# Optimization experiments

Measured on AMD Instinct MI355X. Metric: run time of the kernel, lower is better.

The kernel has to match this reference:

```python
import jax, jax.numpy as jnp
import numpy as np

N_NODES = 50000
N_EDGES = 800000
VOCAB = 500
IN_DIM = 128
HID = 128
OUT_DIM = 64
N_GRAPHS = 512


def setup_inputs() -> dict:
    key = jax.random.key(0)
    ks = jax.random.split(key, 12)
    s = 0.05
    return {
        "emb": jax.random.normal(ks[0], (VOCAB, IN_DIM), jnp.float32) * s,
        "w1a": jax.random.normal(ks[1], (HID, IN_DIM), jnp.float32) * s,
        "b1a": jnp.zeros((HID,), jnp.float32),
        "w1b": jax.random.normal(ks[2], (HID, HID), jnp.float32) * s,
        "b1b": jnp.zeros((HID,), jnp.float32),
        "w2a": jax.random.normal(ks[3], (HID, HID), jnp.float32) * s,
        "b2a": jnp.zeros((HID,), jnp.float32),
        "w2b": jax.random.normal(ks[4], (HID, HID), jnp.float32) * s,
        "b2b": jnp.zeros((HID,), jnp.float32),
        "fc_w": jax.random.normal(ks[5], (OUT_DIM, HID), jnp.float32) * s,
        "fc_b": jnp.zeros((OUT_DIM,), jnp.float32),
        "x_idx": jax.random.randint(ks[6], (N_NODES,), 0, VOCAB, jnp.int32),
        "edge_index": jax.random.randint(ks[7], (2, N_EDGES), 0, N_NODES, jnp.int32),
        "batch": jnp.sort(jax.random.randint(ks[8], (N_NODES,), 0, N_GRAPHS, jnp.int32)),
    }


def gin_conv(x, wa, ba, wb, bb, src, dst):
    # GINConv with eps=0: MLP(x + sum_{j->i} x_j)
    agg = jax.ops.segment_sum(x[src], dst, num_segments=N_NODES)  # [N, d]
    h = x + agg
    h = jax.nn.relu(h @ wa.T + ba)
    return h @ wb.T + bb


def reference(emb, w1a, b1a, w1b, b1b, w2a, b2a, w2b, b2b, fc_w, fc_b,
              x_idx, edge_index, batch):
    src, dst = edge_index[0], edge_index[1]
    x = emb[x_idx]  # [N, IN_DIM] embedding lookup
    x = jax.nn.relu(gin_conv(x, w1a, b1a, w1b, b1b, src, dst))
    x = jax.nn.relu(gin_conv(x, w2a, b2a, w2b, b2b, src, dst))
    # global mean pool over graphs
    sums = jax.ops.segment_sum(x, batch, num_segments=N_GRAPHS)  # [G, HID]
    cnt = jax.ops.segment_sum(jnp.ones((N_NODES,), x.dtype), batch, num_segments=N_GRAPHS)
    pooled = sums / jnp.maximum(cnt, 1.0)[:, None]
    return pooled @ fc_w.T + fc_b  # [G, OUT_DIM]
```

## Files before the change

### kernel.cpp

```cpp
#include <hip/hip_runtime.h>

#define N_NODES 50000
#define N_EDGES 800000
#define DIM 128
#define NGRAPH 512
#define ODIM 64
#define VOCAB 500
#define NBKT 391
#define NB2 128
#define EPB2 (N_EDGES / NB2)
#define CAP 4096

typedef __attribute__((ext_vector_type(8))) short bf16x8;
typedef __attribute__((ext_vector_type(4))) short bf16x4;
typedef __attribute__((ext_vector_type(4))) float f32x4;

__device__ inline unsigned short f2bf(float f) {
  unsigned u = __builtin_bit_cast(unsigned, f);
  return (unsigned short)((u + 0x7fffu + ((u >> 16) & 1u)) >> 16);
}
__device__ inline float bf2f(unsigned short h) {
  unsigned u = ((unsigned)h) << 16;
  return __builtin_bit_cast(float, u);
}

__global__ __launch_bounds__(256) void emb2bf_kernel(
    const float* __restrict__ emb, unsigned short* __restrict__ embb) {
  int i = blockIdx.x * 256 + threadIdx.x;
  if (i >= VOCAB * 16) return;
  const f32x4* src = (const f32x4*)(emb + (size_t)i * 8);
  f32x4 a = src[0], b = src[1];
  bf16x8 o;
  #pragma unroll
  for (int e = 0; e < 4; ++e) {
    o[e] = (short)f2bf(a[e]);
    o[4 + e] = (short)f2bf(b[e]);
  }
  *(bf16x8*)(embb + (size_t)i * 8) = o;
}

__global__ __launch_bounds__(256) void w2bf_kernel(
    const float* __restrict__ w1a, const float* __restrict__ w1b,
    const float* __restrict__ w2a, const float* __restrict__ w2b,
    unsigned short* __restrict__ wbf) {
  int u = blockIdx.x * 256 + threadIdx.x;
  if (u >= 4 * 2048) return;
  int m = u >> 11, loc = u & 2047;
  const float* src = (m == 0) ? w1a : (m == 1) ? w1b : (m == 2) ? w2a : w2b;
  const f32x4* sp = (const f32x4*)(src + (size_t)loc * 8);
  f32x4 a = sp[0], b = sp[1];
  bf16x8 o;
  #pragma unroll
  for (int e = 0; e < 4; ++e) {
    o[e] = (short)f2bf(a[e]);
    o[4 + e] = (short)f2bf(b[e]);
  }
  *(bf16x8*)(wbf + (size_t)u * 8) = o;
}

__global__ __launch_bounds__(512) void bkt_hist_kernel(
    const int* __restrict__ ei, unsigned* __restrict__ HB) {
  __shared__ unsigned cnt[NBKT];
  int t = threadIdx.x, b = blockIdx.x;
  for (int i = t; i < NBKT; i += 512) cnt[i] = 0;
  __syncthreads();
  int base = b * EPB2;
  for (int i = t; i < EPB2; i += 512)
    atomicAdd(&cnt[(unsigned)ei[N_EDGES + base + i] >> 7], 1u);
  __syncthreads();
  for (int i = t; i < NBKT; i += 512) HB[(size_t)b * NBKT + i] = cnt[i];
}

__global__ __launch_bounds__(128) void col_scan_kernel(
    const unsigned* __restrict__ HB, unsigned* __restrict__ OFF,
    unsigned* __restrict__ tot) {
  __shared__ unsigned w0s;
  int k = blockIdx.x, t = threadIdx.x;
  int lane = t & 63, wid = t >> 6;
  unsigned v = HB[(size_t)t * NBKT + k];
  unsigned s = v;
  #pragma unroll
  for (int d = 1; d < 64; d <<= 1) {
    unsigned u = __shfl_up(s, d, 64);
    if (lane >= d) s += u;
  }
  if (wid == 0 && lane == 63) w0s = s;
  __syncthreads();
  unsigned excl = s - v + (wid ? w0s : 0u);
  OFF[(size_t)t * NBKT + k] = excl;
  if (t == 127) tot[k] = excl + v;
}

__global__ __launch_bounds__(512) void base_scan_kernel(
    const unsigned* __restrict__ tot, int* __restrict__ bktbase,
    int* __restrict__ row) {
  __shared__ unsigned wsum[8];
  int t = threadIdx.x;
  int lane = t & 63, wid = t >> 6;
  unsigned v = (t < NBKT) ? tot[t] : 0u;
  unsigned s = v;
  #pragma unroll
  for (int d = 1; d < 64; d <<= 1) {
    unsigned u = __shfl_up(s, d, 64);
    if (lane >= d) s += u;
  }
  if (lane == 63) wsum[wid] = s;
  __syncthreads();
  if (wid == 0) {
    unsigned ws = (lane < 8) ? wsum[lane] : 0u;
    #pragma unroll
    for (int d = 1; d < 8; d <<= 1) {
      unsigned u = __shfl_up(ws, d, 64);
      if (lane >= d) ws += u;
    }
    if (lane < 8) wsum[lane] = ws;
  }
  __syncthreads();
  unsigned excl = s - v + (wid ? wsum[wid - 1] : 0u);
  if (t < NBKT) bktbase[t] = (int)excl;
  if (t == NBKT - 1) {
    bktbase[NBKT] = (int)(excl + v);
    row[N_NODES] = N_EDGES;
  }
}

__global__ __launch_bounds__(512) void bkt_scatter_kernel(
    const int* __restrict__ ei, const unsigned* __restrict__ OFF,
    const int* __restrict__ bktbase, unsigned* __restrict__ eb) {
  __shared__ unsigned cur[NBKT];
  int t = threadIdx.x, b = blockIdx.x;
  for (int i = t; i < NBKT; i += 512)
    cur[i] = OFF[(size_t)b * NBKT + i] + (unsigned)bktbase[i];
  __syncthreads();
  int base = b * EPB2;
  for (int i = t; i < EPB2; i += 512) {
    int s = ei[base + i];
    unsigned d = (unsigned)ei[N_EDGES + base + i];
    unsigned pos = atomicAdd(&cur[d >> 7], 1u);
    eb[pos] = ((d & 127u) << 16) | (unsigned)s;
  }
}

__global__ __launch_bounds__(256) void sort_bucket_kernel(
    const unsigned* __restrict__ eb, const int* __restrict__ bktbase,
    int* __restrict__ srt, int* __restrict__ row) {
  __shared__ unsigned stage[CAP];
  __shared__ unsigned short sorted[CAP];
  __shared__ unsigned hist[128], excl[128], cur[128];
  __shared__ unsigned wtot;
  int t = threadIdx.x, bkt = blockIdx.x;
  int base = bktbase[bkt], end = bktbase[bkt + 1];
  int cnt = end - base;
  if (cnt > CAP) cnt = CAP;
  if (t < 128) hist[t] = 0;
  __syncthreads();
  for (int i = t; i < cnt; i += 256) {
    unsigned e = eb[base + i];
    stage[i] = e;
    atomicAdd(&hist[e >> 16], 1u);
  }
  __syncthreads();
  if (t < 128) {
    int lane = t & 63;
    unsigned v = hist[t], s = v;
    #pragma unroll
    for (int d = 1; d < 64; d <<= 1) {
      unsigned u = __shfl_up(s, d, 64);
      if (lane >= d) s += u;
    }
    if (t == 63) wtot = s;
    excl[t] = s - v;
  }
  __syncthreads();
  if (t < 128) {
    unsigned e0 = excl[t] + (t >= 64 ? wtot : 0u);
    cur[t] = e0;
    int n = bkt * 128 + t;
    if (n < N_NODES) row[n] = base + (int)e0;
  }
  __syncthreads();
  for (int i = t; i < cnt; i += 256) {
    unsigned e = stage[i];
    unsigned r = atomicAdd(&cur[e >> 16], 1u);
    sorted[r] = (unsigned short)(e & 0xFFFFu);
  }
  __syncthreads();
  for (int i = t; i < cnt; i += 256) srt[base + i] = (int)sorted[i];
}

__global__ __launch_bounds__(256) void agg_emb_kernel(
    const unsigned short* __restrict__ embb, const int* __restrict__ xidx,
    const int* __restrict__ row, const int* __restrict__ srt,
    unsigned short* __restrict__ xa) {
  int n = blockIdx.x * 16 + (threadIdx.x >> 4);
  int c = threadIdx.x & 15;
  int lo = row[n], hi = row[n + 1];
  bf16x8 sv = *(const bf16x8*)(embb + (size_t)xidx[n] * DIM + c * 8);
  float a[8];
  #pragma unroll
  for (int e = 0; e < 8; ++e) a[e] = bf2f((unsigned short)sv[e]);
  int k = lo;
  for (; k + 8 <= hi; k += 8) {
    bf16x8 w[8];
    #pragma unroll
    for (int q = 0; q < 8; ++q)
      w[q] = *(const bf16x8*)(embb + (size_t)xidx[srt[k + q]] * DIM + c * 8);
    #pragma unroll
    for (int q = 0; q < 8; ++q)
      #pragma unroll
      for (int e = 0; e < 8; ++e) a[e] += bf2f((unsigned short)w[q][e]);
  }
  for (; k + 2 <= hi; k += 2) {
    bf16x8 w0 = *(const bf16x8*)(embb + (size_t)xidx[srt[k]] * DIM + c * 8);
    bf16x8 w1 = *(const bf16x8*)(embb + (size_t)xidx[srt[k + 1]] * DIM + c * 8);
    #pragma unroll
    for (int e = 0; e < 8; ++e)
      a[e] += bf2f((unsigned short)w0[e]) + bf2f((unsigned short)w1[e]);
  }
  if (k < hi) {
    bf16x8 w = *(const bf16x8*)(embb + (size_t)xidx[srt[k]] * DIM + c * 8);
    #pragma unroll
    for (int e = 0; e < 8; ++e) a[e] += bf2f((unsigned short)w[e]);
  }
  bf16x8 o;
  #pragma unroll
  for (int e = 0; e < 8; ++e) o[e] = (short)f2bf(a[e]);
  *(bf16x8*)(xa + (size_t)n * DIM + c * 8) = o;
}

__global__ __launch_bounds__(256) void agg_x_kernel(
    const unsigned short* __restrict__ x, const int* __restrict__ row,
    const int* __restrict__ srt, unsigned short* __restrict__ xa) {
  int n = blockIdx.x * 16 + (threadIdx.x >> 4);
  int c = threadIdx.x & 15;
  int lo = row[n], hi = row[n + 1];
  bf16x8 sv = *(const bf16x8*)(x + (size_t)n * DIM + c * 8);
  float a[8];
  #pragma unroll
  for (int e = 0; e < 8; ++e) a[e] = bf2f((unsigned short)sv[e]);
  int k = lo;
  for (; k + 8 <= hi; k += 8) {
    bf16x8 w[8];
    #pragma unroll
    for (int q = 0; q < 8; ++q)
      w[q] = *(const bf16x8*)(x + (size_t)srt[k + q] * DIM + c * 8);
    #pragma unroll
    for (int q = 0; q < 8; ++q)
      #pragma unroll
      for (int e = 0; e < 8; ++e) a[e] += bf2f((unsigned short)w[q][e]);
  }
  for (; k + 2 <= hi; k += 2) {
    bf16x8 w0 = *(const bf16x8*)(x + (size_t)srt[k] * DIM + c * 8);
    bf16x8 w1 = *(const bf16x8*)(x + (size_t)srt[k + 1] * DIM + c * 8);
    #pragma unroll
    for (int e = 0; e < 8; ++e)
      a[e] += bf2f((unsigned short)w0[e]) + bf2f((unsigned short)w1[e]);
  }
  if (k < hi) {
    bf16x8 w = *(const bf16x8*)(x + (size_t)srt[k] * DIM + c * 8);
    #pragma unroll
    for (int e = 0; e < 8; ++e) a[e] += bf2f((unsigned short)w[e]);
  }
  bf16x8 o;
  #pragma unroll
  for (int e = 0; e < 8; ++e) o[e] = (short)f2bf(a[e]);
  *(bf16x8*)(xa + (size_t)n * DIM + c * 8) = o;
}

__global__ __launch_bounds__(256) void mlp_mfma_kernel(
    const unsigned short* __restrict__ xa,
    const unsigned short* __restrict__ wabf, const float* __restrict__ ba,
    const unsigned short* __restrict__ wbbf, const float* __restrict__ bb,
    unsigned short* __restrict__ xout) {
  __shared__ short Xs[64 * 128];
  __shared__ short Hs[64 * 128];
  int t = threadIdx.x;
  int lane = t & 63;
  int w = t >> 6;
  int jq = w * 32;
  int l15 = lane & 15;
  int lg = lane >> 4;
  int nbase = blockIdx.x * 64;

  bf16x8 waf[2][4], wbf[2][4];
  #pragma unroll
  for (int jm = 0; jm < 2; ++jm) {
    int jrow = jq + jm * 16 + l15;
    #pragma unroll
    for (int ks = 0; ks < 4; ++ks) {
      int k0 = ks * 32 + lg * 8;
      waf[jm][ks] = *(const bf16x8*)(wabf + (size_t)jrow * DIM + k0);
      wbf[jm][ks] = *(const bf16x8*)(wbbf + (size_t)jrow * DIM + k0);
    }
  }
  f32x4 ba_r[2], bb_r[2];
  #pragma unroll
  for (int jm = 0; jm < 2; ++jm) {
    ba_r[jm] = *(const f32x4*)(ba + jq + jm * 16 + lg * 4);
    bb_r[jm] = *(const f32x4*)(bb + jq + jm * 16 + lg * 4);
  }

  {
    int r = t >> 2;
    int cb = (t & 3) * 4;
    int node = nbase + r;
    #pragma unroll
    for (int i = 0; i < 4; ++i) {
      int chunk = cb + i;
      bf16x8 v = {0, 0, 0, 0, 0, 0, 0, 0};
      if (node < N_NODES)
        v = *(const bf16x8*)(xa + (size_t)node * DIM + chunk * 8);
      *(bf16x8*)&Xs[r * 128 + ((chunk ^ (r & 7)) << 3)] = v;
    }
  }
  __syncthreads();

  #pragma unroll
  for (int nt = 0; nt < 4; ++nt) {
    int rrow = nt * 16 + l15;
    bf16x8 xf[4];
    #pragma unroll
    for (int ks = 0; ks < 4; ++ks) {
      int chunk = ks * 4 + lg;
      xf[ks] = *(const bf16x8*)&Xs[rrow * 128 + ((chunk ^ (rrow & 7)) << 3)];
    }
    #pragma unroll
    for (int jm = 0; jm < 2; ++jm) {
      f32x4 acc = ba_r[jm];
      #pragma unroll
      for (int ks = 0; ks < 4; ++ks)
        acc = __builtin_amdgcn_mfma_f32_16x16x32_bf16(waf[jm][ks], xf[ks], acc, 0, 0, 0);
      int hnode = nt * 16 + l15;
      int cbase = jq + jm * 16 + lg * 4;
      unsigned p0 = (unsigned)f2bf(fmaxf(acc[0], 0.f)) |
                    ((unsigned)f2bf(fmaxf(acc[1], 0.f)) << 16);
      unsigned p1 = (unsigned)f2bf(fmaxf(acc[2], 0.f)) |
                    ((unsigned)f2bf(fmaxf(acc[3], 0.f)) << 16);
      unsigned idx = hnode * 128 + (((cbase >> 3) ^ (hnode & 7)) << 3) + (cbase & 7);
      *(uint2*)&Hs[idx] = make_uint2(p0, p1);
    }
  }
  __syncthreads();

  #pragma unroll
  for (int nt = 0; nt < 4; ++nt) {
    int rrow = nt * 16 + l15;
    bf16x8 hf[4];
    #pragma unroll
    for (int ks = 0; ks < 4; ++ks) {
      int chunk = ks * 4 + lg;
      hf[ks] = *(const bf16x8*)&Hs[rrow * 128 + ((chunk ^ (rrow & 7)) << 3)];
    }
    #pragma unroll
    for (int jm = 0; jm < 2; ++jm) {
      f32x4 acc = bb_r[jm];
      #pragma unroll
      for (int ks = 0; ks < 4; ++ks)
        acc = __builtin_amdgcn_mfma_f32_16x16x32_bf16(wbf[jm][ks], hf[ks], acc, 0, 0, 0);
      int node = nbase + nt * 16 + l15;
      if (node < N_NODES) {
        bf16x4 o;
        #pragma unroll
        for (int e = 0; e < 4; ++e) o[e] = (short)f2bf(fmaxf(acc[e], 0.f));
        *(bf16x4*)(xout + (size_t)node * DIM + jq + jm * 16 + lg * 4) = o;
      }
    }
  }
}

#define PP 132
__global__ __launch_bounds__(256) void pool_fc_kernel(
    const unsigned short* __restrict__ x, const int* __restrict__ batch,
    const float* __restrict__ fcw, const float* __restrict__ fcb,
    float* __restrict__ out) {
  int g = blockIdx.x, t = threadIdx.x;
  __shared__ float part[16 * PP];
  __shared__ float pooled[DIM];
  __shared__ int sbound[2];
  if (t < 2) {
    int target = g + t;
    int lo = 0, hi = N_NODES;
    while (lo < hi) {
      int m = (lo + hi) >> 1;
      if (batch[m] < target) lo = m + 1; else hi = m;
    }
    sbound[t] = lo;
  }
  __syncthreads();
  int lo = sbound[0], hi = sbound[1];
  int r = t >> 4, c = t & 15;
  float acc[8] = {0.f, 0.f, 0.f, 0.f, 0.f, 0.f, 0.f, 0.f};
  for (int nn = lo + r; nn < hi; nn += 16) {
    bf16x8 v = *(const bf16x8*)(x + (size_t)nn * DIM + c * 8);
    #pragma unroll
    for (int e = 0; e < 8; ++e) acc[e] += bf2f((unsigned short)v[e]);
  }
  #pragma unroll
  for (int e = 0; e < 8; ++e) part[r * PP + c * 8 + e] = acc[e];
  __syncthreads();
  if (t < DIM) {
    float s = 0.f;
    #pragma unroll
    for (int rr = 0; rr < 16; ++rr) s += part[rr * PP + t];
    pooled[t] = s / fmaxf((float)(hi - lo), 1.0f);
  }
  __syncthreads();
  if (t < ODIM) {
    float a = fcb[t];
    const float* wr = fcw + (size_t)t * DIM;
    #pragma unroll 8
    for (int h = 0; h < DIM; ++h) a += pooled[h] * wr[h];
    out[(size_t)g * ODIM + t] = a;
  }
}

extern "C" void kernel_launch(void* const* d_in, const int* in_sizes, int n_in,
                              void* d_out, int out_size, void* d_ws, size_t ws_size,
                              hipStream_t stream) {
  const float* emb  = (const float*)d_in[0];
  const float* w1a  = (const float*)d_in[1];
  const float* b1a  = (const float*)d_in[2];
  const float* w1b  = (const float*)d_in[3];
  const float* b1b  = (const float*)d_in[4];
  const float* w2a  = (const float*)d_in[5];
  const float* b2a  = (const float*)d_in[6];
  const float* w2b  = (const float*)d_in[7];
  const float* b2b  = (const float*)d_in[8];
  const float* fcw  = (const float*)d_in[9];
  const float* fcb  = (const float*)d_in[10];
  const int*   xidx = (const int*)d_in[11];
  const int*   ei   = (const int*)d_in[12];
  const int*   batch= (const int*)d_in[13];
  float* out = (float*)d_out;

  size_t featb = (size_t)N_NODES * DIM * sizeof(unsigned short);
  char* ws = (char*)d_ws;
  unsigned short* B1 = (unsigned short*)ws;
  unsigned short* B2 = (unsigned short*)(ws + featb);
  char* p = ws + 2 * featb;
  unsigned short* embb = (unsigned short*)p;  p += (VOCAB * DIM * 2 + 15) / 16 * 16;
  unsigned short* wbf  = (unsigned short*)p;  p += (4 * DIM * DIM * 2 + 15) / 16 * 16;
  int* row  = (int*)p;      p += ((N_NODES + 1) * 4 + 15) / 16 * 16;
  int* bktbase = (int*)p;   p += ((NBKT + 1) * 4 + 15) / 16 * 16;
  unsigned* HB  = (unsigned*)p;  p += (size_t)NB2 * NBKT * 4;
  unsigned* OFF = (unsigned*)p;  p += (size_t)NB2 * NBKT * 4;
  unsigned* tot = (unsigned*)p;  p += (NBKT * 4 + 15) / 16 * 16;
  unsigned* eb  = (unsigned*)p;  p += (size_t)N_EDGES * 4;
  int* srt  = (int*)p;

  const unsigned short* w1abf = wbf;
  const unsigned short* w1bbf = wbf + DIM * DIM;
  const unsigned short* w2abf = wbf + 2 * DIM * DIM;
  const unsigned short* w2bbf = wbf + 3 * DIM * DIM;

  emb2bf_kernel<<<(VOCAB * 16 + 255) / 256, 256, 0, stream>>>(emb, embb);
  w2bf_kernel<<<32, 256, 0, stream>>>(w1a, w1b, w2a, w2b, wbf);

  bkt_hist_kernel<<<NB2, 512, 0, stream>>>(ei, HB);
  col_scan_kernel<<<NBKT, 128, 0, stream>>>(HB, OFF, tot);
  base_scan_kernel<<<1, 512, 0, stream>>>(tot, bktbase, row);
  bkt_scatter_kernel<<<NB2, 512, 0, stream>>>(ei, OFF, bktbase, eb);
  sort_bucket_kernel<<<NBKT, 256, 0, stream>>>(eb, bktbase, srt, row);

  agg_emb_kernel<<<N_NODES / 16, 256, 0, stream>>>(embb, xidx, row, srt, B1);
  mlp_mfma_kernel<<<(N_NODES + 63) / 64, 256, 0, stream>>>(B1, w1abf, b1a, w1bbf, b1b, B2);

  agg_x_kernel<<<N_NODES / 16, 256, 0, stream>>>(B2, row, srt, B1);
  mlp_mfma_kernel<<<(N_NODES + 63) / 64, 256, 0, stream>>>(B1, w2abf, b2a, w2bbf, b2b, B2);

  pool_fc_kernel<<<NGRAPH, 256, 0, stream>>>(B2, batch, fcw, fcb, out);
}
```

Baseline: 134.6 us.

## Fuse prep and scan kernels, recompute scans in-kernel, double MLP node tile

Merges the embedding and weight bf16 conversion kernels into a single launch. It removes the column-scan and base-scan kernels by having each scatter block and each sort block recompute bucket prefix sums straight from the histogram, which cuts two launches and their intermediate buffers. In exchange every block now reads the full histogram column, adding redundant global reads. The MLP kernel also processes two 64-node tiles per block so the weight fragments loaded into registers are reused across more nodes, at the cost of fewer blocks.

```diff
diff --git a/kernel.cpp b/kernel.cpp
--- a/kernel.cpp
+++ b/kernel.cpp
@@ -24,38 +24,33 @@
   return __builtin_bit_cast(float, u);
 }
 
-__global__ __launch_bounds__(256) void emb2bf_kernel(
-    const float* __restrict__ emb, unsigned short* __restrict__ embb) {
-  int i = blockIdx.x * 256 + threadIdx.x;
-  if (i >= VOCAB * 16) return;
-  const f32x4* src = (const f32x4*)(emb + (size_t)i * 8);
-  f32x4 a = src[0], b = src[1];
+__global__ __launch_bounds__(256) void prep_kernel(
+    const float* __restrict__ emb,
+    const float* __restrict__ w1a, const float* __restrict__ w1b,
+    const float* __restrict__ w2a, const float* __restrict__ w2b,
+    unsigned short* __restrict__ embb, unsigned short* __restrict__ wbf) {
+  int u = blockIdx.x * 256 + threadIdx.x;
+  const float* src;
+  unsigned short* dst;
+  if (u < VOCAB * 16) {
+    src = emb + (size_t)u * 8;
+    dst = embb + (size_t)u * 8;
+  } else {
+    int v = u - VOCAB * 16;
+    if (v >= 4 * 2048) return;
+    int m = v >> 11, loc = v & 2047;
+    const float* w = (m == 0) ? w1a : (m == 1) ? w1b : (m == 2) ? w2a : w2b;
+    src = w + (size_t)loc * 8;
+    dst = wbf + (size_t)v * 8;
+  }
+  f32x4 a = ((const f32x4*)src)[0], b = ((const f32x4*)src)[1];
   bf16x8 o;
   #pragma unroll
   for (int e = 0; e < 4; ++e) {
     o[e] = (short)f2bf(a[e]);
     o[4 + e] = (short)f2bf(b[e]);
   }
-  *(bf16x8*)(embb + (size_t)i * 8) = o;
-}
-
-__global__ __launch_bounds__(256) void w2bf_kernel(
-    const float* __restrict__ w1a, const float* __restrict__ w1b,
-    const float* __restrict__ w2a, const float* __restrict__ w2b,
-    unsigned short* __restrict__ wbf) {
-  int u = blockIdx.x * 256 + threadIdx.x;
-  if (u >= 4 * 2048) return;
-  int m = u >> 11, loc = u & 2047;
-  const float* src = (m == 0) ? w1a : (m == 1) ? w1b : (m == 2) ? w2a : w2b;
-  const f32x4* sp = (const f32x4*)(src + (size_t)loc * 8);
-  f32x4 a = sp[0], b = sp[1];
-  bf16x8 o;
-  #pragma unroll
-  for (int e = 0; e < 4; ++e) {
-    o[e] = (short)f2bf(a[e]);
-    o[4 + e] = (short)f2bf(b[e]);
-  }
-  *(bf16x8*)(wbf + (size_t)u * 8) = o;
+  *(bf16x8*)dst = o;
 }
 
 __global__ __launch_bounds__(512) void bkt_hist_kernel(
@@ -71,34 +66,65 @@
   for (int i = t; i < NBKT; i += 512) HB[(size_t)b * NBKT + i] = cnt[i];
 }
 
-__global__ __launch_bounds__(128) void col_scan_kernel(
-    const unsigned* __restrict__ HB, unsigned* __restrict__ OFF,
-    unsigned* __restrict__ tot) {
-  __shared__ unsigned w0s;
-  int k = blockIdx.x, t = threadIdx.x;
+__global__ __launch_bounds__(512) void bkt_scatter_kernel(
+    const int* __restrict__ ei, const unsigned* __restrict__ HB,
+    unsigned* __restrict__ eb) {
+  __shared__ unsigned cur[NBKT];
+  __shared__ unsigned wsum[8];
+  int t = threadIdx.x, b = blockIdx.x;
   int lane = t & 63, wid = t >> 6;
-  unsigned v = HB[(size_t)t * NBKT + k];
-  unsigned s = v;
+  unsigned pre = 0, tot = 0;
+  if (t < NBKT) {
+    for (int bb = 0; bb < NB2; ++bb) {
+      unsigned h = HB[(size_t)bb * NBKT + t];
+      pre += (bb < b) ? h : 0u;
+      tot += h;
+    }
+  }
+  unsigned s = tot;
   #pragma unroll
   for (int d = 1; d < 64; d <<= 1) {
     unsigned u = __shfl_up(s, d, 64);
     if (lane >= d) s += u;
   }
-  if (wid == 0 && lane == 63) w0s = s;
-  __syncthreads();
-  unsigned excl = s - v + (wid ? w0s : 0u);
-  OFF[(size_t)t * NBKT + k] = excl;
-  if (t == 127) tot[k] = excl + v;
-}
-
-__global__ __launch_bounds__(512) void base_scan_kernel(
-    const unsigned* __restrict__ tot, int* __restrict__ bktbase,
-    int* __restrict__ row) {
-  __shared__ unsigned wsum[8];
-  int t = threadIdx.x;
+  if (lane == 63) wsum[wid] = s;
+  __syncthreads();
+  if (wid == 0) {
+    unsigned ws = (lane < 8) ? wsum[lane] : 0u;
+    #pragma unroll
+    for (int d = 1; d < 8; d <<= 1) {
+      unsigned u = __shfl_up(ws, d, 64);
+      if (lane >= d) ws += u;
+    }
+    if (lane < 8) wsum[lane] = ws;
+  }
+  __syncthreads();
+  unsigned base = s - tot + (wid ? wsum[wid - 1] : 0u);
+  if (t < NBKT) cur[t] = base + pre;
+  __syncthreads();
+  int ebase = b * EPB2;
+  for (int i = t; i < EPB2; i += 512) {
+    int sn = ei[ebase + i];
+    unsigned d = (unsigned)ei[N_EDGES + ebase + i];
+    unsigned pos = atomicAdd(&cur[d >> 7], 1u);
+    eb[pos] = ((d & 127u) << 16) | (unsigned)sn;
+  }
+}
+
+__global__ __launch_bounds__(512) void sort_bucket_kernel(
+    const unsigned* __restrict__ HB, const unsigned* __restrict__ eb,
+    int* __restrict__ srt, int* __restrict__ row) {
+  __shared__ unsigned stage[CAP];
+  __shared__ unsigned short sorted[CAP];
+  __shared__ unsigned hist[128], cur[128];
+  __shared__ unsigned wtot, wsum[8];
+  __shared__ int sbound[2];
+  int t = threadIdx.x, bkt = blockIdx.x;
   int lane = t & 63, wid = t >> 6;
-  unsigned v = (t < NBKT) ? tot[t] : 0u;
-  unsigned s = v;
+  unsigned tot = 0;
+  if (t < NBKT)
+    for (int bb = 0; bb < NB2; ++bb) tot += HB[(size_t)bb * NBKT + t];
+  unsigned s = tot;
   #pragma unroll
   for (int d = 1; d < 64; d <<= 1) {
     unsigned u = __shfl_up(s, d, 64);
@@ -116,76 +142,45 @@
     if (lane < 8) wsum[lane] = ws;
   }
   __syncthreads();
-  unsigned excl = s - v + (wid ? wsum[wid - 1] : 0u);
-  if (t < NBKT) bktbase[t] = (int)excl;
-  if (t == NBKT - 1) {
-    bktbase[NBKT] = (int)(excl + v);
-    row[N_NODES] = N_EDGES;
-  }
-}
-
-__global__ __launch_bounds__(512) void bkt_scatter_kernel(
-    const int* __restrict__ ei, const unsigned* __restrict__ OFF,
-    const int* __restrict__ bktbase, unsigned* __restrict__ eb) {
-  __shared__ unsigned cur[NBKT];
-  int t = threadIdx.x, b = blockIdx.x;
-  for (int i = t; i < NBKT; i += 512)
-    cur[i] = OFF[(size_t)b * NBKT + i] + (unsigned)bktbase[i];
-  __syncthreads();
-  int base = b * EPB2;
-  for (int i = t; i < EPB2; i += 512) {
-    int s = ei[base + i];
-    unsigned d = (unsigned)ei[N_EDGES + base + i];
-    unsigned pos = atomicAdd(&cur[d >> 7], 1u);
-    eb[pos] = ((d & 127u) << 16) | (unsigned)s;
-  }
-}
-
-__global__ __launch_bounds__(256) void sort_bucket_kernel(
-    const unsigned* __restrict__ eb, const int* __restrict__ bktbase,
-    int* __restrict__ srt, int* __restrict__ row) {
-  __shared__ unsigned stage[CAP];
-  __shared__ unsigned short sorted[CAP];
-  __shared__ unsigned hist[128], excl[128], cur[128];
-  __shared__ unsigned wtot;
-  int t = threadIdx.x, bkt = blockIdx.x;
-  int base = bktbase[bkt], end = bktbase[bkt + 1];
-  int cnt = end - base;
+  unsigned base = s - tot + (wid ? wsum[wid - 1] : 0u);
+  if (t == bkt) { sbound[0] = (int)base; sbound[1] = (int)(base + tot); }
+  if (t < 128) hist[t] = 0;
+  if (bkt == 0 && t == 0) row[N_NODES] = N_EDGES;
+  __syncthreads();
+  int bs = sbound[0];
+  int cnt = sbound[1] - bs;
   if (cnt > CAP) cnt = CAP;
-  if (t < 128) hist[t] = 0;
-  __syncthreads();
-  for (int i = t; i < cnt; i += 256) {
-    unsigned e = eb[base + i];
+  for (int i = t; i < cnt; i += 512) {
+    unsigned e = eb[bs + i];
     stage[i] = e;
     atomicAdd(&hist[e >> 16], 1u);
   }
   __syncthreads();
   if (t < 128) {
-    int lane = t & 63;
-    unsigned v = hist[t], s = v;
+    unsigned v = hist[t], ss = v;
     #pragma unroll
     for (int d = 1; d < 64; d <<= 1) {
-      unsigned u = __shfl_up(s, d, 64);
-      if (lane >= d) s += u;
-    }
-    if (t == 63) wtot = s;
-    excl[t] = s - v;
+      unsigned u = __shfl_up(ss, d, 64);
+      if (lane >= d) ss += u;
+    }
+    if (t == 63) wtot = ss;
+    cur[t] = ss - v;
   }
   __syncthreads();
   if (t < 128) {
-    unsigned e0 = excl[t] + (t >= 64 ? wtot : 0u);
+    unsigned e0 = cur[t] + (t >= 64 ? wtot : 0u);
     cur[t] = e0;
     int n = bkt * 128 + t;
-    if (n < N_NODES) row[n] = base + (int)e0;
-  }
-  __syncthreads();
-  for (int i = t; i < cnt; i += 256) {
+    if (n < N_NODES) row[n] = bs + (int)e0;
+  }
+  __syncthreads();
+  for (int i = t; i < cnt; i += 512) {
     unsigned e = stage[i];
     unsigned r = atomicAdd(&cur[e >> 16], 1u);
     sorted[r] = (unsigned short)(e & 0xFFFFu);
   }
   __syncthreads();
-  for (int i = t; i < cnt; i += 256) srt[base + i] = (int)sorted[i];
+  for (int i = t; i < cnt; i += 512) srt[bs + i] = (int)sorted[i];
 }
 
 __global__ __launch_bounds__(256) void agg_emb_kernel(
@@ -280,7 +275,6 @@
   int jq = w * 32;
   int l15 = lane & 15;
   int lg = lane >> 4;
-  int nbase = blockIdx.x * 64;
 
   bf16x8 waf[2][4], wbf[2][4];
   #pragma unroll
@@ -300,71 +294,76 @@
     bb_r[jm] = *(const f32x4*)(bb + jq + jm * 16 + lg * 4);
   }
 
-  {
-    int r = t >> 2;
-    int cb = (t & 3) * 4;
-    int node = nbase + r;
-    #pragma unroll
-    for (int i = 0; i < 4; ++i) {
-      int chunk = cb + i;
-      bf16x8 v = {0, 0, 0, 0, 0, 0, 0, 0};
-      if (node < N_NODES)
-        v = *(const bf16x8*)(xa + (size_t)node * DIM + chunk * 8);
-      *(bf16x8*)&Xs[r * 128 + ((chunk ^ (r & 7)) << 3)] = v;
-    }
-  }
-  __syncthreads();
-
-  #pragma unroll
-  for (int nt = 0; nt < 4; ++nt) {
-    int rrow = nt * 16 + l15;
-    bf16x8 xf[4];
-    #pragma unroll
-    for (int ks = 0; ks < 4; ++ks) {
-      int chunk = ks * 4 + lg;
-      xf[ks] = *(const bf16x8*)&Xs[rrow * 128 + ((chunk ^ (rrow & 7)) << 3)];
-    }
-    #pragma unroll
-    for (int jm = 0; jm < 2; ++jm) {
-      f32x4 acc = ba_r[jm];
-      #pragma unroll
-      for (int ks = 0; ks < 4; ++ks)
-        acc = __builtin_amdgcn_mfma_f32_16x16x32_bf16(waf[jm][ks], xf[ks], acc, 0, 0, 0);
-      int hnode = nt * 16 + l15;
-      int cbase = jq + jm * 16 + lg * 4;
-      unsigned p0 = (unsigned)f2bf(fmaxf(acc[0], 0.f)) |
-                    ((unsigned)f2bf(fmaxf(acc[1], 0.f)) << 16);
-      unsigned p1 = (unsigned)f2bf(fmaxf(acc[2], 0.f)) |
-                    ((unsigned)f2bf(fmaxf(acc[3], 0.f)) << 16);
-      unsigned idx = hnode * 128 + (((cbase >> 3) ^ (hnode & 7)) << 3) + (cbase & 7);
-      *(uint2*)&Hs[idx] = make_uint2(p0, p1);
-    }
-  }
-  __syncthreads();
-
-  #pragma unroll
-  for (int nt = 0; nt < 4; ++nt) {
-    int rrow = nt * 16 + l15;
-    bf16x8 hf[4];
-    #pragma unroll
-    for (int ks = 0; ks < 4; ++ks) {
-      int chunk = ks * 4 + lg;
-      hf[ks] = *(const bf16x8*)&Hs[rrow * 128 + ((chunk ^ (rrow & 7)) << 3)];
-    }
-    #pragma unroll
-    for (int jm = 0; jm < 2; ++jm) {
-      f32x4 acc = bb_r[jm];
-      #pragma unroll
-      for (int ks = 0; ks < 4; ++ks)
-        acc = __builtin_amdgcn_mfma_f32_16x16x32_bf16(wbf[jm][ks], hf[ks], acc, 0, 0, 0);
-      int node = nbase + nt * 16 + l15;
-      if (node < N_NODES) {
-        bf16x4 o;
+  for (int half = 0; half < 2; ++half) {
+    int nbase = blockIdx.x * 128 + half * 64;
+
+    {
+      int r = t >> 2;
+      int cb = (t & 3) * 4;
+      int node = nbase + r;
+      #pragma unroll
+      for (int i = 0; i < 4; ++i) {
+        int chunk = cb + i;
+        bf16x8 v = {0, 0, 0, 0, 0, 0, 0, 0};
+        if (node < N_NODES)
+          v = *(const bf16x8*)(xa + (size_t)node * DIM + chunk * 8);
+        *(bf16x8*)&Xs[r * 128 + ((chunk ^ (r & 7)) << 3)] = v;
+      }
+    }
+    __syncthreads();
+
+    #pragma unroll
+    for (int nt = 0; nt < 4; ++nt) {
+      int rrow = nt * 16 + l15;
+      bf16x8 xf[4];
+      #pragma unroll
+      for (int ks = 0; ks < 4; ++ks) {
+        int chunk = ks * 4 + lg;
+        xf[ks] = *(const bf16x8*)&Xs[rrow * 128 + ((chunk ^ (rrow & 7)) << 3)];
+      }
+      #pragma unroll
+      for (int jm = 0; jm < 2; ++jm) {
+        f32x4 acc = ba_r[jm];
         #pragma unroll
-        for (int e = 0; e < 4; ++e) o[e] = (short)f2bf(fmaxf(acc[e], 0.f));
-        *(bf16x4*)(xout + (size_t)node * DIM + jq + jm * 16 + lg * 4) = o;
+        for (int ks = 0; ks < 4; ++ks)
+          acc = __builtin_amdgcn_mfma_f32_16x16x32_bf16(waf[jm][ks], xf[ks], acc, 0, 0, 0);
+        int hnode = nt * 16 + l15;
+        int cbase = jq + jm * 16 + lg * 4;
+        unsigned p0 = (unsigned)f2bf(fmaxf(acc[0], 0.f)) |
+                      ((unsigned)f2bf(fmaxf(acc[1], 0.f)) << 16);
+        unsigned p1 = (unsigned)f2bf(fmaxf(acc[2], 0.f)) |
+                      ((unsigned)f2bf(fmaxf(acc[3], 0.f)) << 16);
+        unsigned idx = hnode * 128 + (((cbase >> 3) ^ (hnode & 7)) << 3) + (cbase & 7);
+        *(uint2*)&Hs[idx] = make_uint2(p0, p1);
       }
     }
+    __syncthreads();
+
+    #pragma unroll
+    for (int nt = 0; nt < 4; ++nt) {
+      int rrow = nt * 16 + l15;
+      bf16x8 hf[4];
+      #pragma unroll
+      for (int ks = 0; ks < 4; ++ks) {
+        int chunk = ks * 4 + lg;
+        hf[ks] = *(const bf16x8*)&Hs[rrow * 128 + ((chunk ^ (rrow & 7)) << 3)];
+      }
+      #pragma unroll
+      for (int jm = 0; jm < 2; ++jm) {
+        f32x4 acc = bb_r[jm];
+        #pragma unroll
+        for (int ks = 0; ks < 4; ++ks)
+          acc = __builtin_amdgcn_mfma_f32_16x16x32_bf16(wbf[jm][ks], hf[ks], acc, 0, 0, 0);
+        int node = nbase + nt * 16 + l15;
+        if (node < N_NODES) {
+          bf16x4 o;
+          #pragma unroll
+          for (int e = 0; e < 4; ++e) o[e] = (short)f2bf(fmaxf(acc[e], 0.f));
+          *(bf16x4*)(xout + (size_t)node * DIM + jq + jm * 16 + lg * 4) = o;
+        }
+      }
+    }
+    __syncthreads();
   }
 }
 
@@ -441,10 +440,7 @@
   unsigned short* embb = (unsigned short*)p;  p += (VOCAB * DIM * 2 + 15) / 16 * 16;
   unsigned short* wbf  = (unsigned short*)p;  p += (4 * DIM * DIM * 2 + 15) / 16 * 16;
   int* row  = (int*)p;      p += ((N_NODES + 1) * 4 + 15) / 16 * 16;
-  int* bktbase = (int*)p;   p += ((NBKT + 1) * 4 + 15) / 16 * 16;
   unsigned* HB  = (unsigned*)p;  p += (size_t)NB2 * NBKT * 4;
-  unsigned* OFF = (unsigned*)p;  p += (size_t)NB2 * NBKT * 4;
-  unsigned* tot = (unsigned*)p;  p += (NBKT * 4 + 15) / 16 * 16;
   unsigned* eb  = (unsigned*)p;  p += (size_t)N_EDGES * 4;
   int* srt  = (int*)p;
 
@@ -453,20 +449,18 @@
   const unsigned short* w2abf = wbf + 2 * DIM * DIM;
   const unsigned short* w2bbf = wbf + 3 * DIM * DIM;
 
-  emb2bf_kernel<<<(VOCAB * 16 + 255) / 256, 256, 0, stream>>>(emb, embb);
-  w2bf_kernel<<<32, 256, 0, stream>>>(w1a, w1b, w2a, w2b, wbf);
+  prep_kernel<<<(VOCAB * 16 + 4 * 2048 + 255) / 256, 256, 0, stream>>>(
+      emb, w1a, w1b, w2a, w2b, embb, wbf);
 
   bkt_hist_kernel<<<NB2, 512, 0, stream>>>(ei, HB);
-  col_scan_kernel<<<NBKT, 128, 0, stream>>>(HB, OFF, tot);
-  base_scan_kernel<<<1, 512, 0, stream>>>(tot, bktbase, row);
-  bkt_scatter_kernel<<<NB2, 512, 0, stream>>>(ei, OFF, bktbase, eb);
-  sort_bucket_kernel<<<NBKT, 256, 0, stream>>>(eb, bktbase, srt, row);
+  bkt_scatter_kernel<<<NB2, 512, 0, stream>>>(ei, HB, eb);
+  sort_bucket_kernel<<<NBKT, 512, 0, stream>>>(HB, eb, srt, row);
 
   agg_emb_kernel<<<N_NODES / 16, 256, 0, stream>>>(embb, xidx, row, srt, B1);
-  mlp_mfma_kernel<<<(N_NODES + 63) / 64, 256, 0, stream>>>(B1, w1abf, b1a, w1bbf, b1b, B2);
+  mlp_mfma_kernel<<<(N_NODES + 127) / 128, 256, 0, stream>>>(B1, w1abf, b1a, w1bbf, b1b, B2);
 
   agg_x_kernel<<<N_NODES / 16, 256, 0, stream>>>(B2, row, srt, B1);
-  mlp_mfma_kernel<<<(N_NODES + 63) / 64, 256, 0, stream>>>(B1, w2abf, b2a, w2bbf, b2b, B2);
+  mlp_mfma_kernel<<<(N_NODES + 127) / 128, 256, 0, stream>>>(B1, w2abf, b2a, w2bbf, b2b, B2);
 
   pool_fc_kernel<<<NGRAPH, 256, 0, stream>>>(B2, batch, fcw, fcb, out);
 }
```

New measurement: 131.5 us. -2.3%, faster.
